# Optimization experiments

Hardware: AMD Instinct MI355X
Metric: run time of the kernel (lower is better)

## Reference

```python
import jax, jax.numpy as jnp
import numpy as np

B, L, V, E, D, NH, HD, NL = 4, 2048, 32000, 300, 128, 4, 128, 3
D2 = NH * HD  # 512
W = 3  # ring window size (unfold_size)
EPS = 1e-5


def setup_inputs() -> dict:
    key = jax.random.key(0)
    ks = jax.random.split(key, 16)
    s = 0.02
    w = lambda k, shape: (jax.random.normal(k, shape, jnp.float32) * s)
    inp = {
        "tokens": jax.random.randint(ks[0], (B, L), 0, V),
        "mask": jax.random.randint(ks[1], (B, L), 0, 2).astype(jnp.int32),
        "emb_table": w(ks[2], (V, E)),
        "proj_w": w(ks[3], (D, E)),
        "proj_b": jnp.zeros((D,), jnp.float32),
        "ng": jnp.ones((NL, D), jnp.float32),
        "nb": jnp.zeros((NL, D), jnp.float32),
        "rq_w": w(ks[4], (NL, D2, D)), "rq_b": jnp.zeros((NL, D2), jnp.float32),
        "rk_w": w(ks[5], (NL, D2, D)), "rk_b": jnp.zeros((NL, D2), jnp.float32),
        "rv_w": w(ks[6], (NL, D2, D)), "rv_b": jnp.zeros((NL, D2), jnp.float32),
        "ro_w": w(ks[7], (NL, D, D2)), "ro_b": jnp.zeros((NL, D), jnp.float32),
        "sq_w": w(ks[8], (NL, D2, D)), "sq_b": jnp.zeros((NL, D2), jnp.float32),
        "sk_w": w(ks[9], (NL, D2, D)), "sk_b": jnp.zeros((NL, D2), jnp.float32),
        "sv_w": w(ks[10], (NL, D2, D)), "sv_b": jnp.zeros((NL, D2), jnp.float32),
        "so_w": w(ks[11], (NL, D, D2)), "so_b": jnp.zeros((NL, D), jnp.float32),
    }
    return inp


def _layernorm(x, g, b):
    mu = x.mean(-1, keepdims=True)
    var = x.var(-1, keepdims=True)
    return (x - mu) / jnp.sqrt(var + EPS) * g + b


def reference(tokens, mask, emb_table, proj_w, proj_b, ng, nb,
              rq_w, rq_b, rk_w, rk_b, rv_w, rv_b, ro_w, ro_b,
              sq_w, sq_b, sk_w, sk_b, sv_w, sv_b, so_w, so_b):
    b, l = tokens.shape
    pad = (mask == 0)                                        # [B,L] True at padding
    smask = jnp.concatenate([jnp.zeros((b, 1), bool), pad], axis=1)  # [B,L+1]
    x = emb_table[tokens] @ proj_w.T + proj_b                # [B,L,D]
    nodes = x
    relay = x.mean(axis=1)                                   # [B,D]
    r_embs = x                                               # fixed original embeddings
    scale = 1.0 / np.sqrt(HD).astype(np.float32)
    for i in range(NL):
        nx = _layernorm(nodes, ng[i], nb[i])
        # ----- MSA1: ring (windowed) attention + relay extras -----
        q = (nx @ rq_w[i].T + rq_b[i]).reshape(b, l, NH, HD)
        k = (nx @ rk_w[i].T + rk_b[i]).reshape(b, l, NH, HD)
        v = (nx @ rv_w[i].T + rv_b[i]).reshape(b, l, NH, HD)
        relay_bc = jnp.broadcast_to(relay[:, None, :], (b, l, D))
        ax = jnp.stack([r_embs, relay_bc], axis=2)           # [B,L,2,D]
        ak = (ax @ rk_w[i].T + rk_b[i]).reshape(b, l, 2, NH, HD)
        av = (ax @ rv_w[i].T + rv_b[i]).reshape(b, l, 2, NH, HD)
        kp = jnp.pad(k, ((0, 0), (1, 1), (0, 0), (0, 0)))    # zero pad like F.unfold
        vp = jnp.pad(v, ((0, 0), (1, 1), (0, 0), (0, 0)))
        kw = jnp.stack([kp[:, u:u + l] for u in range(W)], axis=2)  # [B,L,3,NH,HD]
        vw = jnp.stack([vp[:, u:u + l] for u in range(W)], axis=2)
        kall = jnp.concatenate([kw, ak], axis=2)             # [B,L,5,NH,HD]
        vall = jnp.concatenate([vw, av], axis=2)
        scores = jnp.einsum('blnh,blunh->blun', q, kall) * scale
        alphas = jax.nn.softmax(scores, axis=2)
        att = jnp.einsum('blun,blunh->blnh', alphas, vall).reshape(b, l, D2)
        nodes = nodes + jax.nn.leaky_relu(att @ ro_w[i].T + ro_b[i])
        # ----- MSA2: relay (global) attention over [relay; nodes] -----
        y = jnp.concatenate([relay[:, None, :], nodes], axis=1)      # [B,L+1,D]
        sq = (relay @ sq_w[i].T + sq_b[i]).reshape(b, NH, HD)
        sk = (y @ sk_w[i].T + sk_b[i]).reshape(b, l + 1, NH, HD)
        sv = (y @ sv_w[i].T + sv_b[i]).reshape(b, l + 1, NH, HD)
        pre = jnp.einsum('bnh,blnh->bnl', sq, sk) * scale            # [B,NH,L+1]
        pre = jnp.where(smask[:, None, :], -jnp.inf, pre)
        al = jax.nn.softmax(pre, axis=2)
        satt = jnp.einsum('bnl,blnh->bnh', al, sv).reshape(b, D2)
        relay = jax.nn.leaky_relu(satt @ so_w[i].T + so_b[i])
        nodes = jnp.where(pad[:, :, None], 0.0, nodes)
    return relay  # a_v: [B, d_model] (use_attention=False path)
```

## Files before the change

### kernel.cpp

```cpp
#include <hip/hip_runtime.h>
#include <hip/hip_bf16.h>

constexpr int B = 4, L = 2048, E = 300, D = 128, NH = 4, HD = 128, NL = 3, D2 = 512;
constexpr float EPS = 1e-5f;
constexpr float SCALE = 0.08838834764831843f;
constexpr int NCH = 64;

typedef unsigned int uint_t;
typedef unsigned short u16;
typedef short bf16x8 __attribute__((ext_vector_type(8)));
typedef float f32x4 __attribute__((ext_vector_type(4)));

__device__ __forceinline__ u16 f2bf(float f) {
  union { float f; uint_t i; } x; x.f = f;
  uint_t r = x.i + 0x7fffu + ((x.i >> 16) & 1u);
  return (u16)(r >> 16);
}
__device__ __forceinline__ uint_t packbf(float a, float b) {
  return (uint_t)f2bf(a) | ((uint_t)f2bf(b) << 16);
}
__device__ __forceinline__ float bf2f(u16 u) {
  union { uint_t i; float f; } x; x.i = ((uint_t)u) << 16; return x.f;
}
__device__ __forceinline__ float2 bf2x2(uint_t u) {
  union { uint_t i; float f; } a, b;
  a.i = (u & 0xffffu) << 16; b.i = u & 0xffff0000u;
  return make_float2(a.f, b.f);
}
struct f8 { float v[8]; };
__device__ __forceinline__ f8 unpack8(uint4 u) {
  f8 r;
  float2 a = bf2x2(u.x); r.v[0] = a.x; r.v[1] = a.y;
  float2 b = bf2x2(u.y); r.v[2] = b.x; r.v[3] = b.y;
  float2 c = bf2x2(u.z); r.v[4] = c.x; r.v[5] = c.y;
  float2 d = bf2x2(u.w); r.v[6] = d.x; r.v[7] = d.y;
  return r;
}

struct WCArgs { const float* s[4]; u16* d[4]; };
__global__ __launch_bounds__(256) void wconv(WCArgs wa) {
  int ti = blockIdx.y;
  const float* s = wa.s[ti]; u16* dd = wa.d[ti];
  int i = (blockIdx.x * 256 + threadIdx.x) * 4;
  float4 f = *(const float4*)(s + i);
  *(uint2*)(dd + i) = make_uint2(packbf(f.x, f.y), packbf(f.z, f.w));
}

struct GDesc { const u16* A; const u16* W; const float* bias; u16* outb; };
struct GArgs { GDesc d[5]; };
struct PArgs {
  const float* rel;
  const float* rkw; const float* rkb;
  const float* rvw; const float* rvb;
  const float* sqw; const float* sqb;
  const float* skw; const float* skb;
  float* relay_k; float* relay_v;
  float* u; float* cvec;
};
constexpr int NPROJ = 24;

__global__ __launch_bounds__(256) void gemm_qkv(GArgs ga, PArgs pa, int N) {
  int bid = blockIdx.x;
  int t = threadIdx.x;
  if (bid < NPROJ) {
    __shared__ float rel[D];
    __shared__ float sql2[2][HD];
    __shared__ float credp[4];
    int b = bid / 6, j = bid % 6;
    if (t < D) rel[t] = pa.rel[(size_t)b * D + t];
    __syncthreads();
    const float4* r4 = (const float4*)rel;
    if (j < 4) {
      int which = j >> 1;
      int n = (j & 1) * 256 + t;
      const float* W = which ? pa.rvw : pa.rkw;
      float acc = (which ? pa.rvb : pa.rkb)[n];
      const float4* w4 = (const float4*)(W + (size_t)n * D);
#pragma unroll 8
      for (int i = 0; i < D / 4; i++) {
        float4 w = w4[i], r = r4[i];
        acc += w.x * r.x + w.y * r.y + w.z * r.z + w.w * r.w;
      }
      (which ? pa.relay_v : pa.relay_k)[(size_t)b * D2 + n] = acc;
    } else {
      int hh = t >> 7, th = t & 127;
      int n = (j - 4) * 2 + hh;
      int nh = n * HD + th;
      float acc = pa.sqb[nh];
      const float4* w4 = (const float4*)(pa.sqw + (size_t)nh * D);
#pragma unroll 8
      for (int i = 0; i < D / 4; i++) {
        float4 w = w4[i], r = r4[i];
        acc += w.x * r.x + w.y * r.y + w.z * r.z + w.w * r.w;
      }
      sql2[hh][th] = acc;
      __syncthreads();
      float cp = acc * pa.skb[nh];
#pragma unroll
      for (int o = 1; o < 64; o <<= 1) cp += __shfl_xor(cp, o, 64);
      if ((t & 63) == 0) credp[t >> 6] = cp;
      float a0 = 0.f, a1 = 0.f, a2 = 0.f, a3 = 0.f;
      const float* wp = pa.skw + (size_t)(n * HD) * D + th;
      for (int hx = 0; hx < HD; hx += 4) {
        a0 += sql2[hh][hx] * wp[(size_t)hx * D];
        a1 += sql2[hh][hx + 1] * wp[(size_t)(hx + 1) * D];
        a2 += sql2[hh][hx + 2] * wp[(size_t)(hx + 2) * D];
        a3 += sql2[hh][hx + 3] * wp[(size_t)(hx + 3) * D];
      }
      pa.u[((size_t)b * NH + n) * D + th] = (a0 + a1 + a2 + a3) * SCALE;
      __syncthreads();
      if (th == 0) pa.cvec[b * NH + n] = (credp[2 * hh] + credp[2 * hh + 1]) * SCALE;
    }
    return;
  }
  __shared__ u16 As[128][136];
  __shared__ u16 Ws[128][136];
  int g = bid - NPROJ;
  int bm = g & 63;
  int y = g >> 6;
  int di = y >> 2, bn = y & 3;
  GDesc d = ga.d[di];
  const int rowA = bm * 128, rowW = bn * 128;

  f32x4 acc[4][4];
#pragma unroll
  for (int i = 0; i < 4; i++)
#pragma unroll
    for (int j = 0; j < 4; j++)
      acc[i][j] = (f32x4){0.f, 0.f, 0.f, 0.f};

  const int r = t >> 1, c0 = (t & 1) * 64;
  const int wid = t >> 6;
  const int wm = (wid & 1) * 64, wn = (wid >> 1) * 64;
  const int lr = t & 15, quad = (t >> 4) & 3;

  const u16* Arow = d.A + (size_t)(rowA + r) * 128;
  const u16* Wrow = d.W + (size_t)(rowW + r) * 128;
  uint4 av_[8], wv_[8];
#pragma unroll
  for (int i = 0; i < 8; i++) {
    av_[i] = *(const uint4*)(Arow + c0 + i * 8);
    wv_[i] = *(const uint4*)(Wrow + c0 + i * 8);
  }
#pragma unroll
  for (int i = 0; i < 8; i++) {
    *(uint4*)&As[r][c0 + i * 8] = av_[i];
    *(uint4*)&Ws[r][c0 + i * 8] = wv_[i];
  }
  __syncthreads();
#pragma unroll
  for (int ks = 0; ks < 4; ks++) {
    bf16x8 af[4], bfr[4];
#pragma unroll
    for (int mt = 0; mt < 4; mt++)
      af[mt] = *(const bf16x8*)&As[wm + mt * 16 + lr][ks * 32 + quad * 8];
#pragma unroll
    for (int nt = 0; nt < 4; nt++)
      bfr[nt] = *(const bf16x8*)&Ws[wn + nt * 16 + lr][ks * 32 + quad * 8];
#pragma unroll
    for (int mt = 0; mt < 4; mt++)
#pragma unroll
      for (int nt = 0; nt < 4; nt++)
        acc[mt][nt] = __builtin_amdgcn_mfma_f32_16x16x32_bf16(af[mt], bfr[nt], acc[mt][nt], 0, 0, 0);
  }
  __syncthreads();
#pragma unroll
  for (int nt = 0; nt < 4; nt++) {
    int colL = wn + nt * 16 + lr;
    float bv = d.bias[rowW + colL];
#pragma unroll
    for (int mt = 0; mt < 4; mt++) {
#pragma unroll
      for (int rr = 0; rr < 4; rr++) {
        int rowL = wm + mt * 16 + quad * 4 + rr;
        As[rowL][colL] = f2bf(acc[mt][nt][rr] + bv);
      }
    }
  }
  __syncthreads();
#pragma unroll
  for (int rep = 0; rep < 8; rep++) {
    int lin = rep * 256 + t;
    int rowL = lin >> 4, colL = (lin & 15) * 8;
    uint4 v = *(const uint4*)&As[rowL][colL];
    *(uint4*)&d.outb[(size_t)(rowA + rowL) * N + rowW + colL] = v;
  }
}

__global__ __launch_bounds__(256) void gemm_embed_ln(
    const float* __restrict__ emb, const float* __restrict__ W,
    const float* __restrict__ bias, const int* __restrict__ gather,
    const float* __restrict__ lng, const float* __restrict__ lnb,
    float* __restrict__ nodes, u16* __restrict__ xb, u16* __restrict__ nxb,
    float* __restrict__ relay) {
  __shared__ u16 As[64][72];
  __shared__ u16 Ws[128][72];
  __shared__ float C[64][132];
  __shared__ float gb[2][D];
  __shared__ float lmu[64], lrs[64];
  int t = threadIdx.x;
  int bm = blockIdx.x;
  const int rowA0 = bm * 64;

  f32x4 acc[2][4];
#pragma unroll
  for (int i = 0; i < 2; i++)
#pragma unroll
    for (int j = 0; j < 4; j++)
      acc[i][j] = (f32x4){0.f, 0.f, 0.f, 0.f};

  const int wid = t >> 6;
  const int wm = (wid & 1) * 32, wn = (wid >> 1) * 64;
  const int lr = t & 15, quad = (t >> 4) & 3;
  const int ra = t >> 2, ca = (t & 3) * 16;
  const int rw = t >> 1, cw = (t & 1) * 32;

  if (t < D) { gb[0][t] = lng[t]; gb[1][t] = lnb[t]; }

  const float* Arow = emb + (size_t)gather[rowA0 + ra] * E;
  const float* Wrow = W + (size_t)rw * E;

  for (int kt = 0; kt < E; kt += 64) {
    __syncthreads();
    bool full = (kt + 64 <= E);
#pragma unroll
    for (int ch = 0; ch < 4; ch++) {
      int c = kt + ca + ch * 4;
      float4 fa;
      if (full) fa = *(const float4*)(Arow + c);
      else {
        fa.x = (c + 0 < E) ? Arow[c + 0] : 0.f;
        fa.y = (c + 1 < E) ? Arow[c + 1] : 0.f;
        fa.z = (c + 2 < E) ? Arow[c + 2] : 0.f;
        fa.w = (c + 3 < E) ? Arow[c + 3] : 0.f;
      }
      *(uint2*)&As[ra][ca + ch * 4] = make_uint2(packbf(fa.x, fa.y), packbf(fa.z, fa.w));
    }
#pragma unroll
    for (int ch = 0; ch < 8; ch++) {
      int c = kt + cw + ch * 4;
      float4 fw;
      if (full) fw = *(const float4*)(Wrow + c);
      else {
        fw.x = (c + 0 < E) ? Wrow[c + 0] : 0.f;
        fw.y = (c + 1 < E) ? Wrow[c + 1] : 0.f;
        fw.z = (c + 2 < E) ? Wrow[c + 2] : 0.f;
        fw.w = (c + 3 < E) ? Wrow[c + 3] : 0.f;
      }
      *(uint2*)&Ws[rw][cw + ch * 4] = make_uint2(packbf(fw.x, fw.y), packbf(fw.z, fw.w));
    }
    __syncthreads();
#pragma unroll
    for (int ks = 0; ks < 2; ks++) {
      bf16x8 af[2], bfr[4];
#pragma unroll
      for (int mt = 0; mt < 2; mt++)
        af[mt] = *(const bf16x8*)&As[wm + mt * 16 + lr][ks * 32 + quad * 8];
#pragma unroll
      for (int nt = 0; nt < 4; nt++)
        bfr[nt] = *(const bf16x8*)&Ws[wn + nt * 16 + lr][ks * 32 + quad * 8];
#pragma unroll
      for (int mt = 0; mt < 2; mt++)
#pragma unroll
        for (int nt = 0; nt < 4; nt++)
          acc[mt][nt] = __builtin_amdgcn_mfma_f32_16x16x32_bf16(af[mt], bfr[nt], acc[mt][nt], 0, 0, 0);
    }
  }
#pragma unroll
  for (int nt = 0; nt < 4; nt++) {
    int col = wn + nt * 16 + lr;
    float bv = bias[col];
#pragma unroll
    for (int mt = 0; mt < 2; mt++) {
#pragma unroll
      for (int rr = 0; rr < 4; rr++) {
        int row = wm + mt * 16 + quad * 4 + rr;
        C[row][col] = acc[mt][nt][rr] + bv;
      }
    }
  }
  __syncthreads();
  if (t < 64) {
    float s = 0.f, s2 = 0.f;
#pragma unroll 16
    for (int j = 0; j < D; j++) { float v = C[t][j]; s += v; s2 += v * v; }
    float mu = s * (1.0f / D);
    float var = s2 * (1.0f / D) - mu * mu;
    lmu[t] = mu; lrs[t] = rsqrtf(var + EPS);
  }
  __syncthreads();
#pragma unroll
  for (int rep = 0; rep < 8; rep++) {
    int lin = rep * 1024 + t * 4;
    int row = lin >> 7, col = lin & 127;
    float4 v = *(const float4*)&C[row][col];
    size_t g = (size_t)(rowA0 + row) * D + col;
    *(float4*)&nodes[g] = v;
    *(uint2*)&xb[g] = make_uint2(packbf(v.x, v.y), packbf(v.z, v.w));
    float mu = lmu[row], rs = lrs[row];
    float o0 = (v.x - mu) * rs * gb[0][col] + gb[1][col];
    float o1 = (v.y - mu) * rs * gb[0][col + 1] + gb[1][col + 1];
    float o2 = (v.z - mu) * rs * gb[0][col + 2] + gb[1][col + 2];
    float o3 = (v.w - mu) * rs * gb[0][col + 3] + gb[1][col + 3];
    *(uint2*)&nxb[g] = make_uint2(packbf(o0, o1), packbf(o2, o3));
  }
  if (t < D) {
    int b = rowA0 >> 11;
    float s = 0.f;
#pragma unroll 16
    for (int r2 = 0; r2 < 64; r2++) s += C[r2][t];
    atomicAdd(&relay[b * D + t], s * (1.0f / L));
  }
}

__global__ __launch_bounds__(256) void gemm_ro_ln(
    const u16* __restrict__ A,
    const u16* __restrict__ W,
    const float* __restrict__ bias,
    const int* __restrict__ mask,
    const float* __restrict__ lng, const float* __restrict__ lnb,
    const float* __restrict__ uvec, const float* __restrict__ cvec,
    float* __restrict__ nodes, u16* __restrict__ nxb,
    float* __restrict__ pm, float* __restrict__ ps, float* __restrict__ pw,
    int do_ln) {
  __shared__ u16 As[32][136];
  __shared__ u16 Ws[128][136];
  __shared__ float C[32][132];
  __shared__ float gb[2][D];
  __shared__ float lmu[32], lrs[32];
  __shared__ float usv[NH][D];
  __shared__ float cv2[NH];
  __shared__ float scs[NH][32];
  __shared__ float esr[NH][32];
  int t = threadIdx.x;
  int bm = blockIdx.x;
  const int rowA0 = bm * 32;
  const int b4 = rowA0 >> 11;
  const int chunk = (rowA0 >> 5) & 63;

  f32x4 acc[4];
#pragma unroll
  for (int j = 0; j < 4; j++) acc[j] = (f32x4){0.f, 0.f, 0.f, 0.f};

  const int wid = t >> 6;
  const int wm = (wid & 1) * 16, wn = (wid >> 1) * 64;
  const int lr = t & 15, quad = (t >> 4) & 3;
  const int ra = t >> 3, ca = (t & 7) * 16;
  const int rw = t >> 1, cw = (t & 1) * 64;

  if (do_ln && t < D) { gb[0][t] = lng[t]; gb[1][t] = lnb[t]; }
#pragma unroll
  for (int rep = 0; rep < 2; rep++) {
    int idx = rep * 256 + t;
    usv[idx >> 7][idx & 127] = uvec[(size_t)b4 * NH * D + idx];
  }
  if (t < NH) cv2[t] = cvec[b4 * NH + t];

  const u16* Arow = A + (size_t)(rowA0 + ra) * 512;
  const u16* Wrow = W + (size_t)rw * 512;

  for (int kt = 0; kt < 512; kt += 128) {
    uint4 a0 = *(const uint4*)(Arow + kt + ca);
    uint4 a1 = *(const uint4*)(Arow + kt + ca + 8);
    uint4 w0 = *(const uint4*)(Wrow + kt + cw);
    uint4 w1 = *(const uint4*)(Wrow + kt + cw + 8);
    uint4 w2 = *(const uint4*)(Wrow + kt + cw + 16);
    uint4 w3 = *(const uint4*)(Wrow + kt + cw + 24);
    uint4 w4 = *(const uint4*)(Wrow + kt + cw + 32);
    uint4 w5 = *(const uint4*)(Wrow + kt + cw + 40);
    uint4 w6 = *(const uint4*)(Wrow + kt + cw + 48);
    uint4 w7 = *(const uint4*)(Wrow + kt + cw + 56);
    __syncthreads();
    *(uint4*)&As[ra][ca] = a0; *(uint4*)&As[ra][ca + 8] = a1;
    *(uint4*)&Ws[rw][cw] = w0; *(uint4*)&Ws[rw][cw + 8] = w1;
    *(uint4*)&Ws[rw][cw + 16] = w2; *(uint4*)&Ws[rw][cw + 24] = w3;
    *(uint4*)&Ws[rw][cw + 32] = w4; *(uint4*)&Ws[rw][cw + 40] = w5;
    *(uint4*)&Ws[rw][cw + 48] = w6; *(uint4*)&Ws[rw][cw + 56] = w7;
    __syncthreads();
#pragma unroll
    for (int ks = 0; ks < 4; ks++) {
      bf16x8 af = *(const bf16x8*)&As[wm + lr][ks * 32 + quad * 8];
      bf16x8 bfr[4];
#pragma unroll
      for (int nt = 0; nt < 4; nt++)
        bfr[nt] = *(const bf16x8*)&Ws[wn + nt * 16 + lr][ks * 32 + quad * 8];
#pragma unroll
      for (int nt = 0; nt < 4; nt++)
        acc[nt] = __builtin_amdgcn_mfma_f32_16x16x32_bf16(af, bfr[nt], acc[nt], 0, 0, 0);
    }
  }
  __syncthreads();
#pragma unroll
  for (int nt = 0; nt < 4; nt++) {
    int col = wn + nt * 16 + lr;
    float bv = bias[col];
#pragma unroll
    for (int rr = 0; rr < 4; rr++) {
      int row = wm + quad * 4 + rr;
      float v = acc[nt][rr] + bv;
      v = (v > 0.f) ? v : 0.01f * v;
      v += nodes[(size_t)(rowA0 + row) * D + col];
      if (mask[rowA0 + row] == 0) v = 0.f;
      C[row][col] = v;
    }
  }
  __syncthreads();
  if (t < 32) {
    float s = 0.f, s2 = 0.f;
#pragma unroll 16
    for (int j = 0; j < D; j++) { float v = C[t][j]; s += v; s2 += v * v; }
    float mu = s * (1.0f / D);
    float var = s2 * (1.0f / D) - mu * mu;
    lmu[t] = mu; lrs[t] = rsqrtf(var + EPS);
  }
  __syncthreads();
#pragma unroll
  for (int rep = 0; rep < 4; rep++) {
    int lin = rep * 1024 + t * 4;
    int row = lin >> 7, col = lin & 127;
    float4 v = *(const float4*)&C[row][col];
    size_t g = (size_t)(rowA0 + row) * D + col;
    *(float4*)&nodes[g] = v;
    if (do_ln) {
      float mu = lmu[row], rs = lrs[row];
      float o0 = (v.x - mu) * rs * gb[0][col] + gb[1][col];
      float o1 = (v.y - mu) * rs * gb[0][col + 1] + gb[1][col + 1];
      float o2 = (v.z - mu) * rs * gb[0][col + 2] + gb[1][col + 2];
      float o3 = (v.w - mu) * rs * gb[0][col + 3] + gb[1][col + 3];
      *(uint2*)&nxb[g] = make_uint2(packbf(o0, o1), packbf(o2, o3));
    }
  }
  {
    int n = wid, lane = t & 63;
    int bn = b4 * NH + n;
    const float2* un = (const float2*)usv[n];
    float2 uv2 = un[lane];
    for (int r2 = 0; r2 < 32; r2++) {
      float2 cc = ((const float2*)&C[r2][0])[lane];
      float p = uv2.x * cc.x + uv2.y * cc.y;
#pragma unroll
      for (int o = 1; o < 64; o <<= 1) p += __shfl_xor(p, o, 64);
      if (lane == 0) {
        float s = p + cv2[n];
        if (mask[rowA0 + r2] == 0) s = -1e30f;
        scs[n][r2] = s;
      }
    }
    float m = -1e30f;
    for (int r2 = 0; r2 < 32; r2++) m = fmaxf(m, scs[n][r2]);
    if (lane < 32) esr[n][lane] = expf(scs[n][lane] - m);
    float sum = 0.f;
    for (int r2 = 0; r2 < 32; r2++) sum += esr[n][r2];
    if (lane == 0) { pm[bn * NCH + chunk] = m; ps[bn * NCH + chunk] = sum; }
    float a0 = 0.f, a1 = 0.f;
    for (int r2 = 0; r2 < 32; r2++) {
      float e = esr[n][r2];
      float2 cc = ((const float2*)&C[r2][0])[lane];
      a0 += e * cc.x; a1 += e * cc.y;
    }
    float* pwp = pw + ((size_t)bn * NCH + chunk) * D + 2 * lane;
    pwp[0] = a0; pwp[1] = a1;
  }
}

__global__ __launch_bounds__(256) void ring_attn_kernel(
    const u16* __restrict__ q, const u16* __restrict__ k, const u16* __restrict__ v,
    const u16* __restrict__ akr, const u16* __restrict__ avr,
    const float* __restrict__ rk, const float* __restrict__ rv,
    u16* __restrict__ att) {
  int wv = threadIdx.x >> 6, lane = threadIdx.x & 63;
  int bl = blockIdx.x * 4 + wv;
  int b = bl >> 11, l = bl & (L - 1);
  size_t rowoff = (size_t)bl * D2 + lane * 8;

  uint4 qd = *(const uint4*)(q + rowoff);
  uint4 kd[5], vd[5];
  bool valid[3];
#pragma unroll
  for (int u = 0; u < 3; u++) {
    int ll = l + u - 1;
    valid[u] = (ll >= 0 && ll < L);
    size_t off = ((size_t)b * L + ll) * D2 + lane * 8;
    if (valid[u]) { kd[u] = *(const uint4*)(k + off); vd[u] = *(const uint4*)(v + off); }
    else { kd[u] = make_uint4(0, 0, 0, 0); vd[u] = make_uint4(0, 0, 0, 0); }
  }
  kd[3] = *(const uint4*)(akr + rowoff);
  vd[3] = *(const uint4*)(avr + rowoff);
  size_t rb = (size_t)b * D2 + lane * 8;
  float4 rk0 = *(const float4*)(rk + rb), rk1 = *(const float4*)(rk + rb + 4);
  float4 rv0 = *(const float4*)(rv + rb), rv1 = *(const float4*)(rv + rb + 4);

  f8 qf = unpack8(qd);
  f8 kf[5], vf[5];
#pragma unroll
  for (int u = 0; u < 4; u++) { kf[u] = unpack8(kd[u]); vf[u] = unpack8(vd[u]); }
  kf[4].v[0] = rk0.x; kf[4].v[1] = rk0.y; kf[4].v[2] = rk0.z; kf[4].v[3] = rk0.w;
  kf[4].v[4] = rk1.x; kf[4].v[5] = rk1.y; kf[4].v[6] = rk1.z; kf[4].v[7] = rk1.w;
  vf[4].v[0] = rv0.x; vf[4].v[1] = rv0.y; vf[4].v[2] = rv0.z; vf[4].v[3] = rv0.w;
  vf[4].v[4] = rv1.x; vf[4].v[5] = rv1.y; vf[4].v[6] = rv1.z; vf[4].v[7] = rv1.w;

  float s[5];
#pragma unroll
  for (int u = 0; u < 5; u++) {
    float p = 0.f;
#pragma unroll
    for (int j = 0; j < 8; j++) p += qf.v[j] * kf[u].v[j];
#pragma unroll
    for (int o = 1; o < 16; o <<= 1) p += __shfl_xor(p, o, 64);
    s[u] = p * SCALE;
  }
  float m = s[0];
#pragma unroll
  for (int u = 1; u < 5; u++) m = fmaxf(m, s[u]);
  float e[5], sum = 0.f;
#pragma unroll
  for (int u = 0; u < 5; u++) { e[u] = expf(s[u] - m); sum += e[u]; }
  float inv = 1.0f / sum;
  float o[8];
#pragma unroll
  for (int j = 0; j < 8; j++) {
    float a = 0.f;
#pragma unroll
    for (int u = 0; u < 5; u++) a += e[u] * vf[u].v[j];
    o[j] = a * inv;
  }
  uint4 od;
  od.x = packbf(o[0], o[1]); od.y = packbf(o[2], o[3]);
  od.z = packbf(o[4], o[5]); od.w = packbf(o[6], o[7]);
  *(uint4*)(att + rowoff) = od;
}

__global__ __launch_bounds__(512) void relay_combine(
    const float* __restrict__ pm, const float* __restrict__ ps,
    const float* __restrict__ pw,
    const float* __restrict__ relay_entry,
    const float* __restrict__ uvec_in, const float* __restrict__ cvec_in,
    const float* __restrict__ svw, const float* __restrict__ svb,
    const float* __restrict__ sow, const float* __restrict__ sob,
    float* __restrict__ relay_out) {
  __shared__ float rel0[D];
  __shared__ float wpart[8];
  __shared__ float ecs[NH][NCH];
  __shared__ float wsum[NH][D];
  __shared__ float satts[D2];
  __shared__ float rred[4][D];
  int b = blockIdx.x, t = threadIdx.x;
  int n = t >> 7, h = t & 127;
  int w = t >> 6, lane = t & 63;
  if (t < D) rel0[t] = relay_entry[(size_t)b * D + t];
  __syncthreads();
  float p = uvec_in[((size_t)b * NH + n) * D + h] * rel0[h];
#pragma unroll
  for (int o = 1; o < 64; o <<= 1) p += __shfl_xor(p, o, 64);
  if (lane == 0) wpart[w] = p;
  __syncthreads();
  float s0 = wpart[2 * n] + wpart[2 * n + 1] + cvec_in[b * NH + n];
  int c = h & 63;
  float pmv = pm[(b * NH + n) * NCH + c];
  float m = fmaxf(pmv, s0);
#pragma unroll
  for (int o = 1; o < 64; o <<= 1) m = fmaxf(m, __shfl_xor(m, o, 64));
  float ec = expf(pmv - m);
  if (h < 64) ecs[n][h] = ec;
  float sc = ps[(b * NH + n) * NCH + c] * ec;
#pragma unroll
  for (int o = 1; o < 64; o <<= 1) sc += __shfl_xor(sc, o, 64);
  float e0 = expf(s0 - m);
  float invS = 1.0f / (e0 + sc);
  __syncthreads();
  float acc = e0 * rel0[h];
  const float* pwp = pw + ((size_t)(b * NH + n) * NCH) * D + h;
#pragma unroll 8
  for (int cc = 0; cc < NCH; cc++) acc += ecs[n][cc] * pwp[(size_t)cc * D];
  wsum[n][h] = acc * invS;
  __syncthreads();
  {
    float a = svb[t];
    const float4* wp = (const float4*)(svw + (size_t)t * D);
    const float4* wl = (const float4*)wsum[n];
#pragma unroll 8
    for (int dd = 0; dd < D / 4; dd++) {
      float4 x = wl[dd], y = wp[dd];
      a += x.x * y.x + x.y * y.y + x.z * y.z + x.w * y.w;
    }
    satts[t] = a;
  }
  __syncthreads();
  {
    int part = t >> 7, col = t & 127;
    float a = 0.f;
    const float4* wp = (const float4*)(sow + (size_t)col * D2 + part * 128);
    const float4* a4 = (const float4*)(satts + part * 128);
#pragma unroll 8
    for (int jj = 0; jj < 32; jj++) {
      float4 x = a4[jj], y = wp[jj];
      a += x.x * y.x + x.y * y.y + x.z * y.z + x.w * y.w;
    }
    rred[part][col] = a;
  }
  __syncthreads();
  if (t < D) {
    float a = sob[t] + rred[0][t] + rred[1][t] + rred[2][t] + rred[3][t];
    a = (a > 0.f) ? a : 0.01f * a;
    relay_out[(size_t)b * D + t] = a;
  }
}

extern "C" void kernel_launch(void* const* d_in, const int* in_sizes, int n_in,
                              void* d_out, int out_size, void* d_ws, size_t ws_size,
                              hipStream_t stream) {
  const int* tokens = (const int*)d_in[0];
  const int* mask = (const int*)d_in[1];
  const float* emb = (const float*)d_in[2];
  const float* proj_w = (const float*)d_in[3];
  const float* proj_b = (const float*)d_in[4];
  const float* ng = (const float*)d_in[5];
  const float* nb = (const float*)d_in[6];
  const float* rq_w = (const float*)d_in[7], * rq_b = (const float*)d_in[8];
  const float* rk_w = (const float*)d_in[9], * rk_b = (const float*)d_in[10];
  const float* rv_w = (const float*)d_in[11], * rv_b = (const float*)d_in[12];
  const float* ro_w = (const float*)d_in[13], * ro_b = (const float*)d_in[14];
  const float* sq_w = (const float*)d_in[15], * sq_b = (const float*)d_in[16];
  const float* sk_w = (const float*)d_in[17], * sk_b = (const float*)d_in[18];
  const float* sv_w = (const float*)d_in[19], * sv_b = (const float*)d_in[20];
  const float* so_w = (const float*)d_in[21], * so_b = (const float*)d_in[22];

  const size_t BLD = (size_t)B * L * D;
  const size_t BLD4 = (size_t)B * L * D2;
  const size_t WTEN = (size_t)NL * D * D2;

  float* fp = (float*)d_ws;
  float* nodes = fp;                    fp += BLD;
  float* rbuf0 = fp;                    fp += B * D;
  float* rbuf1 = fp;                    fp += B * D;
  float* relay_k = fp;                  fp += B * D2;
  float* relay_v = fp;                  fp += B * D2;
  float* uv = fp;                       fp += B * NH * D;
  float* cv = fp;                       fp += B * NH;
  float* pm = fp;                       fp += B * NH * NCH;
  float* ps = fp;                       fp += B * NH * NCH;
  float* pw = fp;                       fp += (size_t)B * NH * NCH * D;
  u16* up = (u16*)fp;
  u16* xb = up;                         up += BLD;
  u16* nxb = up;                        up += BLD;
  u16* qb = up;                         up += BLD4;
  u16* kb = up;                         up += BLD4;
  u16* vb = up;                         up += BLD4;
  u16* akb = up;                        up += BLD4;
  u16* avb = up;                        up += BLD4;
  u16* attb = up;                       up += BLD4;
  u16* wb = up;
  u16* wrq = wb, * wrk = wb + WTEN, * wrv = wb + 2 * WTEN, * wro = wb + 3 * WTEN;

  hipMemsetAsync(rbuf0, 0, B * D * sizeof(float), stream);

  {
    WCArgs wa;
    wa.s[0] = rq_w; wa.s[1] = rk_w; wa.s[2] = rv_w; wa.s[3] = ro_w;
    wa.d[0] = wrq; wa.d[1] = wrk; wa.d[2] = wrv; wa.d[3] = wro;
    wconv<<<dim3(WTEN / 1024, 4), 256, 0, stream>>>(wa);
  }
  gemm_embed_ln<<<128, 256, 0, stream>>>(emb, proj_w, proj_b, tokens, ng, nb,
                                         nodes, xb, nxb, rbuf0);

  float* rin[3] = {rbuf0, rbuf1, rbuf0};
  float* rout[3] = {rbuf1, rbuf0, (float*)d_out};

  for (int i = 0; i < NL; i++) {
    const size_t wo = (size_t)i * D * D2;
    const float* rqbi = rq_b + (size_t)i * D2;
    const float* rkbi = rk_b + (size_t)i * D2;
    const float* rvbi = rv_b + (size_t)i * D2;
    const float* robi = ro_b + (size_t)i * D;
    const float* svwi = sv_w + wo, * svbi = sv_b + (size_t)i * D2;
    const float* sowi = so_w + wo, * sobi = so_b + (size_t)i * D;
    const int last = (i == NL - 1);

    {
      GArgs ga = {};
      ga.d[0] = {nxb, wrq + wo, rqbi, qb};
      ga.d[1] = {nxb, wrk + wo, rkbi, kb};
      ga.d[2] = {nxb, wrv + wo, rvbi, vb};
      ga.d[3] = {xb,  wrk + wo, rkbi, akb};
      ga.d[4] = {xb,  wrv + wo, rvbi, avb};
      PArgs pa;
      pa.rel = rin[i];
      pa.rkw = rk_w + wo; pa.rkb = rkbi;
      pa.rvw = rv_w + wo; pa.rvb = rvbi;
      pa.sqw = sq_w + wo; pa.sqb = sq_b + (size_t)i * D2;
      pa.skw = sk_w + wo; pa.skb = sk_b + (size_t)i * D2;
      pa.relay_k = relay_k; pa.relay_v = relay_v; pa.u = uv; pa.cvec = cv;
      gemm_qkv<<<64 * 20 + NPROJ, 256, 0, stream>>>(ga, pa, D2);
    }
    ring_attn_kernel<<<B * L / 4, 256, 0, stream>>>(qb, kb, vb, akb, avb, relay_k, relay_v, attb);
    gemm_ro_ln<<<256, 256, 0, stream>>>(
        attb, wro + wo, robi, mask,
        last ? nullptr : ng + (i + 1) * D, last ? nullptr : nb + (i + 1) * D,
        uv, cv, nodes, nxb, pm, ps, pw, last ? 0 : 1);
    relay_combine<<<B, 512, 0, stream>>>(pm, ps, pw, rin[i], uv, cv,
                                         svwi, svbi, sowi, sobi, rout[i]);
  }
}
```

Baseline: 361.4 us.

## Fuse ring attention into output-projection kernel and relay combine into next QKV launch

The ring-window attention now runs inside the out-projection/LayerNorm kernel, which uses 512 threads per 32-row tile. The attention result is kept in shared memory instead of being written to and re-read from a global bf16 buffer. The relay-combine step for each layer moves into the first blocks of the next layer's QKV launch, and the per-batch relay projections are merged into one block per batch. Together this removes two kernel launches per layer and an intermediate global round trip. The cost is a serialized per-batch tail inside the QKV launch and heavier shared-memory use in the fused kernel.

Result: slower. 377.2 us (+4.4%).

```diff
diff --git a/kernel.cpp b/kernel.cpp
--- a/kernel.cpp
+++ b/kernel.cpp
@@ -18,9 +18,6 @@
 }
 __device__ __forceinline__ uint_t packbf(float a, float b) {
   return (uint_t)f2bf(a) | ((uint_t)f2bf(b) << 16);
-}
-__device__ __forceinline__ float bf2f(u16 u) {
-  union { uint_t i; float f; } x; x.i = ((uint_t)u) << 16; return x.f;
 }
 __device__ __forceinline__ float2 bf2x2(uint_t u) {
   union { uint_t i; float f; } a, b;
@@ -49,73 +46,149 @@
 struct GDesc { const u16* A; const u16* W; const float* bias; u16* outb; };
 struct GArgs { GDesc d[5]; };
 struct PArgs {
-  const float* rel;
+  int mode;
+  const float* rel_in;
+  const float* pm; const float* ps; const float* pw;
+  const float* uprev; const float* cvprev;
+  const float* svw; const float* svb;
+  const float* sow; const float* sob;
+  float* rel_out;
   const float* rkw; const float* rkb;
   const float* rvw; const float* rvb;
   const float* sqw; const float* sqb;
   const float* skw; const float* skb;
-  float* relay_k; float* relay_v;
-  float* u; float* cvec;
+  float* relay_k; float* relay_v; float* u; float* cvec;
 };
-constexpr int NPROJ = 24;
 
 __global__ __launch_bounds__(256) void gemm_qkv(GArgs ga, PArgs pa, int N) {
+  __shared__ u16 As[128][136];
+  __shared__ u16 Ws[128][136];
+  __shared__ float rel[D];
+  __shared__ float sql[D2];
+  __shared__ float wsum2[NH][D];
+  __shared__ float satts[D2];
+  __shared__ float ecs2[256];
   int bid = blockIdx.x;
   int t = threadIdx.x;
-  if (bid < NPROJ) {
-    __shared__ float rel[D];
-    __shared__ float sql2[2][HD];
-    __shared__ float credp[4];
-    int b = bid / 6, j = bid % 6;
-    if (t < D) rel[t] = pa.rel[(size_t)b * D + t];
+  if (bid < B) {
+    int b = bid;
+    int wv = t >> 6, lane = t & 63;
+    if (pa.mode) {
+      if (t < D) rel[t] = pa.rel_in[(size_t)b * D + t];
+      __syncthreads();
+      float2 uu = ((const float2*)(pa.uprev + ((size_t)b * NH + wv) * D))[lane];
+      float2 rr = ((const float2*)rel)[lane];
+      float pdot = uu.x * rr.x + uu.y * rr.y;
+#pragma unroll
+      for (int o = 1; o < 64; o <<= 1) pdot += __shfl_xor(pdot, o, 64);
+      float s0 = pdot + pa.cvprev[b * NH + wv];
+      int bn = b * NH + wv;
+      float pmv = pa.pm[bn * NCH + lane];
+      float m = fmaxf(pmv, s0);
+#pragma unroll
+      for (int o = 1; o < 64; o <<= 1) m = fmaxf(m, __shfl_xor(m, o, 64));
+      float ec = expf(pmv - m);
+      ecs2[wv * 64 + lane] = ec;
+      float sc = pa.ps[bn * NCH + lane] * ec;
+#pragma unroll
+      for (int o = 1; o < 64; o <<= 1) sc += __shfl_xor(sc, o, 64);
+      float e0 = expf(s0 - m);
+      float invS = 1.0f / (e0 + sc);
+      float2 a;
+      a.x = e0 * rel[lane * 2]; a.y = e0 * rel[lane * 2 + 1];
+      const float* pwb = pa.pw + (size_t)bn * NCH * D;
+#pragma unroll 8
+      for (int c = 0; c < NCH; c++) {
+        float2 pw2 = ((const float2*)(pwb + (size_t)c * D))[lane];
+        float e = ecs2[wv * 64 + c];
+        a.x += e * pw2.x; a.y += e * pw2.y;
+      }
+      wsum2[wv][lane * 2] = a.x * invS;
+      wsum2[wv][lane * 2 + 1] = a.y * invS;
+      __syncthreads();
+#pragma unroll
+      for (int pp = 0; pp < 2; pp++) {
+        int nh = pp * 256 + t, n = nh >> 7;
+        float acc = pa.svb[nh];
+        const float4* wp = (const float4*)(pa.svw + (size_t)nh * D);
+        const float4* wl = (const float4*)wsum2[n];
+#pragma unroll 8
+        for (int dd = 0; dd < D / 4; dd++) {
+          float4 x = wl[dd], y = wp[dd];
+          acc += x.x * y.x + x.y * y.y + x.z * y.z + x.w * y.w;
+        }
+        satts[nh] = acc;
+      }
+      __syncthreads();
+      {
+        int part = t >> 7, col = t & 127;
+        float acc = 0.f;
+        const float4* wp = (const float4*)(pa.sow + (size_t)col * D2 + part * 256);
+        const float4* a4 = (const float4*)(satts + part * 256);
+#pragma unroll 8
+        for (int jj = 0; jj < 64; jj++) {
+          float4 x = a4[jj], y = wp[jj];
+          acc += x.x * y.x + x.y * y.y + x.z * y.z + x.w * y.w;
+        }
+        ecs2[part * 128 + col] = acc;
+      }
+      __syncthreads();
+      if (t < D) {
+        float av = pa.sob[t] + ecs2[t] + ecs2[128 + t];
+        av = (av > 0.f) ? av : 0.01f * av;
+        rel[t] = av;
+        pa.rel_out[(size_t)b * D + t] = av;
+      }
+      __syncthreads();
+    } else {
+      if (t < D) rel[t] = pa.rel_in[(size_t)b * D + t];
+      __syncthreads();
+    }
+    const float4* r4 = (const float4*)rel;
+#pragma unroll
+    for (int pp = 0; pp < 2; pp++) {
+      int n = pp * 256 + t;
+      float ak_ = pa.rkb[n], av_ = pa.rvb[n], aq_ = pa.sqb[n];
+      const float4* wk = (const float4*)(pa.rkw + (size_t)n * D);
+      const float4* wv4 = (const float4*)(pa.rvw + (size_t)n * D);
+      const float4* wq = (const float4*)(pa.sqw + (size_t)n * D);
+#pragma unroll 8
+      for (int i2 = 0; i2 < D / 4; i2++) {
+        float4 r = r4[i2];
+        float4 x = wk[i2]; ak_ += x.x * r.x + x.y * r.y + x.z * r.z + x.w * r.w;
+        float4 y = wv4[i2]; av_ += y.x * r.x + y.y * r.y + y.z * r.z + y.w * r.w;
+        float4 z = wq[i2]; aq_ += z.x * r.x + z.y * r.y + z.z * r.z + z.w * r.w;
+      }
+      pa.relay_k[(size_t)b * D2 + n] = ak_;
+      pa.relay_v[(size_t)b * D2 + n] = av_;
+      sql[n] = aq_;
+    }
     __syncthreads();
-    const float4* r4 = (const float4*)rel;
-    if (j < 4) {
-      int which = j >> 1;
-      int n = (j & 1) * 256 + t;
-      const float* W = which ? pa.rvw : pa.rkw;
-      float acc = (which ? pa.rvb : pa.rkb)[n];
-      const float4* w4 = (const float4*)(W + (size_t)n * D);
-#pragma unroll 8
-      for (int i = 0; i < D / 4; i++) {
-        float4 w = w4[i], r = r4[i];
-        acc += w.x * r.x + w.y * r.y + w.z * r.z + w.w * r.w;
-      }
-      (which ? pa.relay_v : pa.relay_k)[(size_t)b * D2 + n] = acc;
-    } else {
-      int hh = t >> 7, th = t & 127;
-      int n = (j - 4) * 2 + hh;
-      int nh = n * HD + th;
-      float acc = pa.sqb[nh];
-      const float4* w4 = (const float4*)(pa.sqw + (size_t)nh * D);
-#pragma unroll 8
-      for (int i = 0; i < D / 4; i++) {
-        float4 w = w4[i], r = r4[i];
-        acc += w.x * r.x + w.y * r.y + w.z * r.z + w.w * r.w;
-      }
-      sql2[hh][th] = acc;
-      __syncthreads();
-      float cp = acc * pa.skb[nh];
+    {
+      float2 sq2 = ((const float2*)(sql + wv * HD))[lane];
+      float2 kb2 = ((const float2*)(pa.skb + wv * HD))[lane];
+      float cp = sq2.x * kb2.x + sq2.y * kb2.y;
 #pragma unroll
       for (int o = 1; o < 64; o <<= 1) cp += __shfl_xor(cp, o, 64);
-      if ((t & 63) == 0) credp[t >> 6] = cp;
+      if (lane == 0) pa.cvec[b * NH + wv] = cp * SCALE;
+    }
+#pragma unroll
+    for (int pp = 0; pp < 2; pp++) {
+      int n = (t >> 7) + 2 * pp, th = t & 127;
       float a0 = 0.f, a1 = 0.f, a2 = 0.f, a3 = 0.f;
       const float* wp = pa.skw + (size_t)(n * HD) * D + th;
-      for (int hx = 0; hx < HD; hx += 4) {
-        a0 += sql2[hh][hx] * wp[(size_t)hx * D];
-        a1 += sql2[hh][hx + 1] * wp[(size_t)(hx + 1) * D];
-        a2 += sql2[hh][hx + 2] * wp[(size_t)(hx + 2) * D];
-        a3 += sql2[hh][hx + 3] * wp[(size_t)(hx + 3) * D];
+      const float* sq = sql + n * HD;
+      for (int h = 0; h < HD; h += 4) {
+        a0 += sq[h] * wp[(size_t)h * D];
+        a1 += sq[h + 1] * wp[(size_t)(h + 1) * D];
+        a2 += sq[h + 2] * wp[(size_t)(h + 2) * D];
+        a3 += sq[h + 3] * wp[(size_t)(h + 3) * D];
       }
       pa.u[((size_t)b * NH + n) * D + th] = (a0 + a1 + a2 + a3) * SCALE;
-      __syncthreads();
-      if (th == 0) pa.cvec[b * NH + n] = (credp[2 * hh] + credp[2 * hh + 1]) * SCALE;
     }
     return;
   }
-  __shared__ u16 As[128][136];
-  __shared__ u16 Ws[128][136];
-  int g = bid - NPROJ;
+  int g = bid - B;
   int bm = g & 63;
   int y = g >> 6;
   int di = y >> 2, bn = y & 3;
@@ -313,8 +386,10 @@
   }
 }
 
-__global__ __launch_bounds__(256) void gemm_ro_ln(
-    const u16* __restrict__ A,
+__global__ __launch_bounds__(512) void attn_ro_ln(
+    const u16* __restrict__ q, const u16* __restrict__ k, const u16* __restrict__ v,
+    const u16* __restrict__ akr, const u16* __restrict__ avr,
+    const float* __restrict__ rkvec, const float* __restrict__ rvvec,
     const u16* __restrict__ W,
     const float* __restrict__ bias,
     const int* __restrict__ mask,
@@ -323,7 +398,7 @@
     float* __restrict__ nodes, u16* __restrict__ nxb,
     float* __restrict__ pm, float* __restrict__ ps, float* __restrict__ pw,
     int do_ln) {
-  __shared__ u16 As[32][136];
+  __shared__ u16 att[32][520];
   __shared__ u16 Ws[128][136];
   __shared__ float C[32][132];
   __shared__ float gb[2][D];
@@ -337,101 +412,146 @@
   const int rowA0 = bm * 32;
   const int b4 = rowA0 >> 11;
   const int chunk = (rowA0 >> 5) & 63;
-
-  f32x4 acc[4];
-#pragma unroll
-  for (int j = 0; j < 4; j++) acc[j] = (f32x4){0.f, 0.f, 0.f, 0.f};
-
-  const int wid = t >> 6;
-  const int wm = (wid & 1) * 16, wn = (wid >> 1) * 64;
+  const int wid = t >> 6, lane = t & 63;
+
+  if (do_ln && t < D) { gb[0][t] = lng[t]; gb[1][t] = lnb[t]; }
+  usv[t >> 7][t & 127] = uvec[(size_t)b4 * NH * D + t];
+  if (t < NH) cv2[t] = cvec[b4 * NH + t];
+
+  {
+    size_t rb = (size_t)b4 * D2 + lane * 8;
+    float4 rk0 = *(const float4*)(rkvec + rb), rk1 = *(const float4*)(rkvec + rb + 4);
+    float4 rv0 = *(const float4*)(rvvec + rb), rv1 = *(const float4*)(rvvec + rb + 4);
+    f8 krel, vrel;
+    krel.v[0] = rk0.x; krel.v[1] = rk0.y; krel.v[2] = rk0.z; krel.v[3] = rk0.w;
+    krel.v[4] = rk1.x; krel.v[5] = rk1.y; krel.v[6] = rk1.z; krel.v[7] = rk1.w;
+    vrel.v[0] = rv0.x; vrel.v[1] = rv0.y; vrel.v[2] = rv0.z; vrel.v[3] = rv0.w;
+    vrel.v[4] = rv1.x; vrel.v[5] = rv1.y; vrel.v[6] = rv1.z; vrel.v[7] = rv1.w;
+#pragma unroll
+    for (int i = 0; i < 4; i++) {
+      int rr_ = wid * 4 + i;
+      int gr = rowA0 + rr_;
+      int l = gr & (L - 1);
+      size_t rowoff = (size_t)gr * D2 + lane * 8;
+      uint4 qd = *(const uint4*)(q + rowoff);
+      uint4 kd[4], vd[4];
+#pragma unroll
+      for (int u2 = 0; u2 < 3; u2++) {
+        int ll = l + u2 - 1;
+        bool ok = (ll >= 0 && ll < L);
+        size_t off = rowoff + (size_t)(u2 - 1) * (size_t)D2;
+        if (ok) { kd[u2] = *(const uint4*)(k + off); vd[u2] = *(const uint4*)(v + off); }
+        else { kd[u2] = make_uint4(0, 0, 0, 0); vd[u2] = make_uint4(0, 0, 0, 0); }
+      }
+      kd[3] = *(const uint4*)(akr + rowoff);
+      vd[3] = *(const uint4*)(avr + rowoff);
+      f8 qf = unpack8(qd);
+      f8 kf[5], vf[5];
+#pragma unroll
+      for (int u2 = 0; u2 < 4; u2++) { kf[u2] = unpack8(kd[u2]); vf[u2] = unpack8(vd[u2]); }
+      kf[4] = krel; vf[4] = vrel;
+      float s[5];
+#pragma unroll
+      for (int u2 = 0; u2 < 5; u2++) {
+        float p = 0.f;
+#pragma unroll
+        for (int j = 0; j < 8; j++) p += qf.v[j] * kf[u2].v[j];
+#pragma unroll
+        for (int o = 1; o < 16; o <<= 1) p += __shfl_xor(p, o, 64);
+        s[u2] = p * SCALE;
+      }
+      float m = s[0];
+#pragma unroll
+      for (int u2 = 1; u2 < 5; u2++) m = fmaxf(m, s[u2]);
+      float e[5], sum = 0.f;
+#pragma unroll
+      for (int u2 = 0; u2 < 5; u2++) { e[u2] = expf(s[u2] - m); sum += e[u2]; }
+      float inv = 1.0f / sum;
+      float o8[8];
+#pragma unroll
+      for (int j = 0; j < 8; j++) {
+        float a = 0.f;
+#pragma unroll
+        for (int u2 = 0; u2 < 5; u2++) a += e[u2] * vf[u2].v[j];
+        o8[j] = a * inv;
+      }
+      uint4 od;
+      od.x = packbf(o8[0], o8[1]); od.y = packbf(o8[2], o8[3]);
+      od.z = packbf(o8[4], o8[5]); od.w = packbf(o8[6], o8[7]);
+      *(uint4*)&att[rr_][lane * 8] = od;
+    }
+  }
+  __syncthreads();
+
+  f32x4 acc[2];
+  acc[0] = (f32x4){0.f, 0.f, 0.f, 0.f};
+  acc[1] = (f32x4){0.f, 0.f, 0.f, 0.f};
+  const int wm = (wid & 1) * 16, wn = (wid >> 1) * 32;
   const int lr = t & 15, quad = (t >> 4) & 3;
-  const int ra = t >> 3, ca = (t & 7) * 16;
-  const int rw = t >> 1, cw = (t & 1) * 64;
-
-  if (do_ln && t < D) { gb[0][t] = lng[t]; gb[1][t] = lnb[t]; }
-#pragma unroll
-  for (int rep = 0; rep < 2; rep++) {
-    int idx = rep * 256 + t;
-    usv[idx >> 7][idx & 127] = uvec[(size_t)b4 * NH * D + idx];
-  }
-  if (t < NH) cv2[t] = cvec[b4 * NH + t];
-
-  const u16* Arow = A + (size_t)(rowA0 + ra) * 512;
+  const int rw = t >> 2, cw = (t & 3) * 32;
   const u16* Wrow = W + (size_t)rw * 512;
-
   for (int kt = 0; kt < 512; kt += 128) {
-    uint4 a0 = *(const uint4*)(Arow + kt + ca);
-    uint4 a1 = *(const uint4*)(Arow + kt + ca + 8);
     uint4 w0 = *(const uint4*)(Wrow + kt + cw);
     uint4 w1 = *(const uint4*)(Wrow + kt + cw + 8);
     uint4 w2 = *(const uint4*)(Wrow + kt + cw + 16);
     uint4 w3 = *(const uint4*)(Wrow + kt + cw + 24);
-    uint4 w4 = *(const uint4*)(Wrow + kt + cw + 32);
-    uint4 w5 = *(const uint4*)(Wrow + kt + cw + 40);
-    uint4 w6 = *(const uint4*)(Wrow + kt + cw + 48);
-    uint4 w7 = *(const uint4*)(Wrow + kt + cw + 56);
     __syncthreads();
-    *(uint4*)&As[ra][ca] = a0; *(uint4*)&As[ra][ca + 8] = a1;
     *(uint4*)&Ws[rw][cw] = w0; *(uint4*)&Ws[rw][cw + 8] = w1;
     *(uint4*)&Ws[rw][cw + 16] = w2; *(uint4*)&Ws[rw][cw + 24] = w3;
-    *(uint4*)&Ws[rw][cw + 32] = w4; *(uint4*)&Ws[rw][cw + 40] = w5;
-    *(uint4*)&Ws[rw][cw + 48] = w6; *(uint4*)&Ws[rw][cw + 56] = w7;
     __syncthreads();
 #pragma unroll
     for (int ks = 0; ks < 4; ks++) {
-      bf16x8 af = *(const bf16x8*)&As[wm + lr][ks * 32 + quad * 8];
-      bf16x8 bfr[4];
-#pragma unroll
-      for (int nt = 0; nt < 4; nt++)
-        bfr[nt] = *(const bf16x8*)&Ws[wn + nt * 16 + lr][ks * 32 + quad * 8];
-#pragma unroll
-      for (int nt = 0; nt < 4; nt++)
-        acc[nt] = __builtin_amdgcn_mfma_f32_16x16x32_bf16(af, bfr[nt], acc[nt], 0, 0, 0);
-    }
-  }
-  __syncthreads();
-#pragma unroll
-  for (int nt = 0; nt < 4; nt++) {
+      bf16x8 af = *(const bf16x8*)&att[wm + lr][kt + ks * 32 + quad * 8];
+#pragma unroll
+      for (int nt = 0; nt < 2; nt++) {
+        bf16x8 bfr = *(const bf16x8*)&Ws[wn + nt * 16 + lr][ks * 32 + quad * 8];
+        acc[nt] = __builtin_amdgcn_mfma_f32_16x16x32_bf16(af, bfr, acc[nt], 0, 0, 0);
+      }
+    }
+  }
+  __syncthreads();
+#pragma unroll
+  for (int nt = 0; nt < 2; nt++) {
     int col = wn + nt * 16 + lr;
     float bv = bias[col];
 #pragma unroll
     for (int rr = 0; rr < 4; rr++) {
       int row = wm + quad * 4 + rr;
-      float v = acc[nt][rr] + bv;
-      v = (v > 0.f) ? v : 0.01f * v;
-      v += nodes[(size_t)(rowA0 + row) * D + col];
-      if (mask[rowA0 + row] == 0) v = 0.f;
-      C[row][col] = v;
+      float vv = acc[nt][rr] + bv;
+      vv = (vv > 0.f) ? vv : 0.01f * vv;
+      vv += nodes[(size_t)(rowA0 + row) * D + col];
+      if (mask[rowA0 + row] == 0) vv = 0.f;
+      C[row][col] = vv;
     }
   }
   __syncthreads();
   if (t < 32) {
     float s = 0.f, s2 = 0.f;
 #pragma unroll 16
-    for (int j = 0; j < D; j++) { float v = C[t][j]; s += v; s2 += v * v; }
+    for (int j = 0; j < D; j++) { float vv = C[t][j]; s += vv; s2 += vv * vv; }
     float mu = s * (1.0f / D);
     float var = s2 * (1.0f / D) - mu * mu;
     lmu[t] = mu; lrs[t] = rsqrtf(var + EPS);
   }
   __syncthreads();
 #pragma unroll
-  for (int rep = 0; rep < 4; rep++) {
-    int lin = rep * 1024 + t * 4;
+  for (int rep = 0; rep < 2; rep++) {
+    int lin = rep * 2048 + t * 4;
     int row = lin >> 7, col = lin & 127;
-    float4 v = *(const float4*)&C[row][col];
+    float4 vv = *(const float4*)&C[row][col];
     size_t g = (size_t)(rowA0 + row) * D + col;
-    *(float4*)&nodes[g] = v;
+    *(float4*)&nodes[g] = vv;
     if (do_ln) {
       float mu = lmu[row], rs = lrs[row];
-      float o0 = (v.x - mu) * rs * gb[0][col] + gb[1][col];
-      float o1 = (v.y - mu) * rs * gb[0][col + 1] + gb[1][col + 1];
-      float o2 = (v.z - mu) * rs * gb[0][col + 2] + gb[1][col + 2];
-      float o3 = (v.w - mu) * rs * gb[0][col + 3] + gb[1][col + 3];
+      float o0 = (vv.x - mu) * rs * gb[0][col] + gb[1][col];
+      float o1 = (vv.y - mu) * rs * gb[0][col + 1] + gb[1][col + 1];
+      float o2 = (vv.z - mu) * rs * gb[0][col + 2] + gb[1][col + 2];
+      float o3 = (vv.w - mu) * rs * gb[0][col + 3] + gb[1][col + 3];
       *(uint2*)&nxb[g] = make_uint2(packbf(o0, o1), packbf(o2, o3));
     }
   }
-  {
-    int n = wid, lane = t & 63;
+  if (wid < 4) {
+    int n = wid;
     int bn = b4 * NH + n;
     const float2* un = (const float2*)usv[n];
     float2 uv2 = un[lane];
@@ -461,73 +581,6 @@
     float* pwp = pw + ((size_t)bn * NCH + chunk) * D + 2 * lane;
     pwp[0] = a0; pwp[1] = a1;
   }
-}
-
-__global__ __launch_bounds__(256) void ring_attn_kernel(
-    const u16* __restrict__ q, const u16* __restrict__ k, const u16* __restrict__ v,
-    const u16* __restrict__ akr, const u16* __restrict__ avr,
-    const float* __restrict__ rk, const float* __restrict__ rv,
-    u16* __restrict__ att) {
-  int wv = threadIdx.x >> 6, lane = threadIdx.x & 63;
-  int bl = blockIdx.x * 4 + wv;
-  int b = bl >> 11, l = bl & (L - 1);
-  size_t rowoff = (size_t)bl * D2 + lane * 8;
-
-  uint4 qd = *(const uint4*)(q + rowoff);
-  uint4 kd[5], vd[5];
-  bool valid[3];
-#pragma unroll
-  for (int u = 0; u < 3; u++) {
-    int ll = l + u - 1;
-    valid[u] = (ll >= 0 && ll < L);
-    size_t off = ((size_t)b * L + ll) * D2 + lane * 8;
-    if (valid[u]) { kd[u] = *(const uint4*)(k + off); vd[u] = *(const uint4*)(v + off); }
-    else { kd[u] = make_uint4(0, 0, 0, 0); vd[u] = make_uint4(0, 0, 0, 0); }
-  }
-  kd[3] = *(const uint4*)(akr + rowoff);
-  vd[3] = *(const uint4*)(avr + rowoff);
-  size_t rb = (size_t)b * D2 + lane * 8;
-  float4 rk0 = *(const float4*)(rk + rb), rk1 = *(const float4*)(rk + rb + 4);
-  float4 rv0 = *(const float4*)(rv + rb), rv1 = *(const float4*)(rv + rb + 4);
-
-  f8 qf = unpack8(qd);
-  f8 kf[5], vf[5];
-#pragma unroll
-  for (int u = 0; u < 4; u++) { kf[u] = unpack8(kd[u]); vf[u] = unpack8(vd[u]); }
-  kf[4].v[0] = rk0.x; kf[4].v[1] = rk0.y; kf[4].v[2] = rk0.z; kf[4].v[3] = rk0.w;
-  kf[4].v[4] = rk1.x; kf[4].v[5] = rk1.y; kf[4].v[6] = rk1.z; kf[4].v[7] = rk1.w;
-  vf[4].v[0] = rv0.x; vf[4].v[1] = rv0.y; vf[4].v[2] = rv0.z; vf[4].v[3] = rv0.w;
-  vf[4].v[4] = rv1.x; vf[4].v[5] = rv1.y; vf[4].v[6] = rv1.z; vf[4].v[7] = rv1.w;
-
-  float s[5];
-#pragma unroll
-  for (int u = 0; u < 5; u++) {
-    float p = 0.f;
-#pragma unroll
-    for (int j = 0; j < 8; j++) p += qf.v[j] * kf[u].v[j];
-#pragma unroll
-    for (int o = 1; o < 16; o <<= 1) p += __shfl_xor(p, o, 64);
-    s[u] = p * SCALE;
-  }
-  float m = s[0];
-#pragma unroll
-  for (int u = 1; u < 5; u++) m = fmaxf(m, s[u]);
-  float e[5], sum = 0.f;
-#pragma unroll
-  for (int u = 0; u < 5; u++) { e[u] = expf(s[u] - m); sum += e[u]; }
-  float inv = 1.0f / sum;
-  float o[8];
-#pragma unroll
-  for (int j = 0; j < 8; j++) {
-    float a = 0.f;
-#pragma unroll
-    for (int u = 0; u < 5; u++) a += e[u] * vf[u].v[j];
-    o[j] = a * inv;
-  }
-  uint4 od;
-  od.x = packbf(o[0], o[1]); od.y = packbf(o[2], o[3]);
-  od.z = packbf(o[4], o[5]); od.w = packbf(o[6], o[7]);
-  *(uint4*)(att + rowoff) = od;
 }
 
 __global__ __launch_bounds__(512) void relay_combine(
@@ -648,7 +701,6 @@
   u16* vb = up;                         up += BLD4;
   u16* akb = up;                        up += BLD4;
   u16* avb = up;                        up += BLD4;
-  u16* attb = up;                       up += BLD4;
   u16* wb = up;
   u16* wrq = wb, * wrk = wb + WTEN, * wrv = wb + 2 * WTEN, * wro = wb + 3 * WTEN;
 
@@ -662,9 +714,6 @@
   }
   gemm_embed_ln<<<128, 256, 0, stream>>>(emb, proj_w, proj_b, tokens, ng, nb,
                                          nodes, xb, nxb, rbuf0);
-
-  float* rin[3] = {rbuf0, rbuf1, rbuf0};
-  float* rout[3] = {rbuf1, rbuf0, (float*)d_out};
 
   for (int i = 0; i < NL; i++) {
     const size_t wo = (size_t)i * D * D2;
@@ -672,8 +721,6 @@
     const float* rkbi = rk_b + (size_t)i * D2;
     const float* rvbi = rv_b + (size_t)i * D2;
     const float* robi = ro_b + (size_t)i * D;
-    const float* svwi = sv_w + wo, * svbi = sv_b + (size_t)i * D2;
-    const float* sowi = so_w + wo, * sobi = so_b + (size_t)i * D;
     const int last = (i == NL - 1);
 
     {
@@ -684,20 +731,30 @@
       ga.d[3] = {xb,  wrk + wo, rkbi, akb};
       ga.d[4] = {xb,  wrv + wo, rvbi, avb};
       PArgs pa;
-      pa.rel = rin[i];
+      pa.mode = (i == 0) ? 0 : 1;
+      pa.rel_in = (i == 2) ? rbuf1 : rbuf0;
+      pa.pm = pm; pa.ps = ps; pa.pw = pw;
+      pa.uprev = uv; pa.cvprev = cv;
+      const size_t wprev = (size_t)(i > 0 ? i - 1 : 0) * D * D2;
+      pa.svw = sv_w + wprev; pa.svb = sv_b + (size_t)(i > 0 ? i - 1 : 0) * D2;
+      pa.sow = so_w + wprev; pa.sob = so_b + (size_t)(i > 0 ? i - 1 : 0) * D;
+      pa.rel_out = (i == 1) ? rbuf1 : rbuf0;
       pa.rkw = rk_w + wo; pa.rkb = rkbi;
       pa.rvw = rv_w + wo; pa.rvb = rvbi;
       pa.sqw = sq_w + wo; pa.sqb = sq_b + (size_t)i * D2;
       pa.skw = sk_w + wo; pa.skb = sk_b + (size_t)i * D2;
       pa.relay_k = relay_k; pa.relay_v = relay_v; pa.u = uv; pa.cvec = cv;
-      gemm_qkv<<<64 * 20 + NPROJ, 256, 0, stream>>>(ga, pa, D2);
-    }
-    ring_attn_kernel<<<B * L / 4, 256, 0, stream>>>(qb, kb, vb, akb, avb, relay_k, relay_v, attb);
-    gemm_ro_ln<<<256, 256, 0, stream>>>(
-        attb, wro + wo, robi, mask,
+      gemm_qkv<<<64 * 20 + B, 256, 0, stream>>>(ga, pa, D2);
+    }
+    attn_ro_ln<<<256, 512, 0, stream>>>(
+        qb, kb, vb, akb, avb, relay_k, relay_v,
+        wro + wo, robi, mask,
         last ? nullptr : ng + (i + 1) * D, last ? nullptr : nb + (i + 1) * D,
         uv, cv, nodes, nxb, pm, ps, pw, last ? 0 : 1);
-    relay_combine<<<B, 512, 0, stream>>>(pm, ps, pw, rin[i], uv, cv,
-                                         svwi, svbi, sowi, sobi, rout[i]);
-  }
-}
+  }
+  const size_t w2 = (size_t)(NL - 1) * D * D2;
+  relay_combine<<<B, 512, 0, stream>>>(pm, ps, pw, rbuf0, uv, cv,
+                                       sv_w + w2, sv_b + (size_t)(NL - 1) * D2,
+                                       so_w + w2, so_b + (size_t)(NL - 1) * D,
+                                       (float*)d_out);
+}
```
